# Performance work log

Measured on AMD Instinct MI355X. Metric: run time of the kernel, lower is better.

Reference implementation:

```python
import jax, jax.numpy as jnp
import numpy as np

EPS = 1e-15
BN_EPS = 1e-5
N_NODES = 50000
N_EDGES = 800000
IN_CH = 32
OUT_CH = 32
DIM = 3


def _gmm_params(key, in_ch, out_ch, K):
    k1, k2, k3, k4 = jax.random.split(key, 4)
    g = jax.random.normal(k1, (in_ch, K * out_ch), jnp.float32) * (1.0 / np.sqrt(in_ch))
    mu = jax.random.normal(k2, (K, DIM), jnp.float32)
    sigma = jax.random.uniform(k3, (K, DIM), jnp.float32, 0.5, 1.5)
    root = jax.random.normal(k4, (in_ch, out_ch), jnp.float32) * (1.0 / np.sqrt(in_ch))
    bias = jnp.zeros((out_ch,), jnp.float32)
    return g, mu, sigma, root, bias


def setup_inputs() -> dict:
    key = jax.random.key(0)
    ks = jax.random.split(key, 12)
    x = jax.random.normal(ks[0], (N_NODES, IN_CH), jnp.float32)
    edge_index = jax.random.randint(ks[1], (2, N_EDGES), 0, N_NODES, jnp.int64)
    edge_attr = jax.random.uniform(ks[2], (N_EDGES, DIM), jnp.float32)
    g1, mu1, sig1, root1, b1 = _gmm_params(ks[3], IN_CH, OUT_CH, 5)
    g2, mu2, sig2, root2, b2 = _gmm_params(ks[4], OUT_CH, OUT_CH, 5)
    gs, mus, sigs, roots, bs = _gmm_params(ks[5], IN_CH, OUT_CH, 1)
    ones = jnp.ones((OUT_CH,), jnp.float32)
    zeros = jnp.zeros((OUT_CH,), jnp.float32)
    return dict(x=x, edge_attr=edge_attr,
                g1=g1, mu1=mu1, sig1=sig1, root1=root1, b1=b1, gam1=ones, bet1=zeros,
                g2=g2, mu2=mu2, sig2=sig2, root2=root2, b2=b2, gam2=ones, bet2=zeros,
                gs=gs, mus=mus, sigs=sigs, roots=roots, bs=bs, gams=ones, bets=zeros,
                edge_index=edge_index)


def gmm_conv(x, edge_index, edge_attr, g, mu, sigma, root, bias, num_nodes):
    # PyG GMMConv (separate kernels=False, aggr='mean', root_weight=True)
    src, dst = edge_index[0], edge_index[1]
    K = mu.shape[0]
    out_ch = root.shape[1]
    # Gaussian mixture weights per edge/kernel: [E, K]
    diff = edge_attr[:, None, :] - mu[None, :, :]               # [E, K, D]
    w = jnp.exp(jnp.sum(-0.5 * diff * diff / (EPS + sigma[None] ** 2), axis=-1))
    # Project and gather source features: [E, K, out]
    xj = (x @ g).reshape(-1, K, out_ch)[src] if False else (x[src] @ g).reshape(-1, K, out_ch)
    msg = jnp.einsum('ek,ekc->ec', w, xj)                        # [E, out]
    agg = jax.ops.segment_sum(msg, dst, num_segments=num_nodes)
    cnt = jax.ops.segment_sum(jnp.ones((msg.shape[0],), msg.dtype), dst, num_segments=num_nodes)
    agg = agg / jnp.maximum(cnt, 1.0)[:, None]                   # mean aggregation
    return agg + x @ root + bias


def batch_norm(x, gamma, beta):
    mean = jnp.mean(x, axis=0)
    var = jnp.var(x, axis=0)
    return gamma * (x - mean) * jax.lax.rsqrt(var + BN_EPS) + beta


def reference(x, edge_attr,
              g1, mu1, sig1, root1, b1, gam1, bet1,
              g2, mu2, sig2, root2, b2, gam2, bet2,
              gs, mus, sigs, roots, bs, gams, bets,
              edge_index):
    n = x.shape[0]
    h = jax.nn.elu(batch_norm(gmm_conv(x, edge_index, edge_attr, g1, mu1, sig1, root1, b1, n), gam1, bet1))
    h = batch_norm(gmm_conv(h, edge_index, edge_attr, g2, mu2, sig2, root2, b2, n), gam2, bet2)
    s = batch_norm(gmm_conv(x, edge_index, edge_attr, gs, mus, sigs, roots, bs, n), gams, bets)
    return jax.nn.elu(h + s)
```

## Files before the change

kernel.cpp:

```cpp
#include <hip/hip_runtime.h>
#include <hip/hip_fp16.h>
#include <math.h>

#define NN 50000
#define NE 800000
#define GEPS 1e-15f
#define BN_EPS 1e-5f
#define NB 196
#define LOG2E 1.4426950408889634f
#define NODES_PER_XCD 6250

typedef _Float16 f16x8 __attribute__((ext_vector_type(8)));
typedef float f32x4 __attribute__((ext_vector_type(4)));

__device__ __forceinline__ float2 h2f(unsigned int u) {
    __half2 h = *reinterpret_cast<const __half2*>(&u);
    return __half22float2(h);
}

__global__ void init_kernel(const float* __restrict__ sig1, const float* __restrict__ mu1,
                            const float* __restrict__ sig2, const float* __restrict__ mu2,
                            const float* __restrict__ sigs, const float* __restrict__ mus,
                            float* __restrict__ gc, int* __restrict__ deg,
                            float* __restrict__ stats) {
    int i = blockIdx.x * blockDim.x + threadIdx.x;
    if (i < NN) deg[i] = 0;
    if (blockIdx.x == 0) {
        int t = threadIdx.x;
        stats[t] = 0.f;
        if (t < 11) {
            const float* sg; const float* mu;
            if (t < 5)       { sg = sig1 + t * 3;       mu = mu1 + t * 3; }
            else if (t < 10) { sg = sig2 + (t - 5) * 3; mu = mu2 + (t - 5) * 3; }
            else             { sg = sigs;               mu = mus; }
            float C = 0.f;
            for (int d = 0; d < 3; d++) {
                float sv = sg[d];
                float iv = -0.5f / (GEPS + sv * sv) * LOG2E;
                float m = mu[d];
                gc[t * 8 + d] = iv;
                gc[t * 8 + 3 + d] = -2.f * iv * m;
                C += iv * m * m;
            }
            gc[t * 8 + 6] = C;
            gc[t * 8 + 7] = 0.f;
        }
    }
}

__global__ void rank_kernel(const int* __restrict__ ei, int* __restrict__ deg,
                            int* __restrict__ rankv) {
    int t = blockIdx.x * blockDim.x + threadIdx.x;
    int e0 = t * 4;
    if (e0 >= NE) return;
    int4 dv = *(const int4*)(ei + NE + e0);
    int4 rv;
    rv.x = atomicAdd(&deg[dv.x], 1);
    rv.y = atomicAdd(&deg[dv.y], 1);
    rv.z = atomicAdd(&deg[dv.z], 1);
    rv.w = atomicAdd(&deg[dv.w], 1);
    *(int4*)(rankv + e0) = rv;
}

__global__ void block_reduce_kernel(const int* __restrict__ deg, int* __restrict__ bsum) {
    __shared__ int sh[256];
    int t = threadIdx.x;
    int i = blockIdx.x * 256 + t;
    sh[t] = (i < NN) ? deg[i] : 0;
    __syncthreads();
    for (int off = 128; off > 0; off >>= 1) {
        if (t < off) sh[t] += sh[t + off];
        __syncthreads();
    }
    if (t == 0) bsum[blockIdx.x] = sh[0];
}

__global__ void scan_partials_kernel(int* __restrict__ bsum) {
    __shared__ int sh[256];
    int t = threadIdx.x;
    int v = (t < NB) ? bsum[t] : 0;
    sh[t] = v;
    __syncthreads();
    for (int off = 1; off < 256; off <<= 1) {
        int u = (t >= off) ? sh[t - off] : 0;
        __syncthreads();
        sh[t] += u;
        __syncthreads();
    }
    if (t < NB) bsum[t] = sh[t] - v;
}

__global__ void block_scan_kernel(const int* __restrict__ deg, const int* __restrict__ bsum,
                                  int* __restrict__ rowstart) {
    __shared__ int sh[256];
    int t = threadIdx.x;
    int i = blockIdx.x * 256 + t;
    int v = (i < NN) ? deg[i] : 0;
    sh[t] = v;
    __syncthreads();
    for (int off = 1; off < 256; off <<= 1) {
        int u = (t >= off) ? sh[t - off] : 0;
        __syncthreads();
        sh[t] += u;
        __syncthreads();
    }
    int excl = sh[t] - v + bsum[blockIdx.x];
    if (i < NN) rowstart[i] = excl;
}

__global__ void scatter_xcd(const int* __restrict__ ei, const int* __restrict__ rankv,
                            const int* __restrict__ rowstart, int* __restrict__ perm) {
    const int g = blockIdx.x & 7;
    const int v = blockIdx.x >> 3;
    const int VB = gridDim.x >> 3;
    const int stride = VB * blockDim.x * 4;
    for (int e0 = (v * blockDim.x + threadIdx.x) * 4; e0 < NE; e0 += stride) {
        int4 dv = *(const int4*)(ei + NE + e0);
        int4 rv = *(const int4*)(rankv + e0);
        if (dv.x / NODES_PER_XCD == g) perm[rowstart[dv.x] + rv.x] = e0;
        if (dv.y / NODES_PER_XCD == g) perm[rowstart[dv.y] + rv.y] = e0 + 1;
        if (dv.z / NODES_PER_XCD == g) perm[rowstart[dv.z] + rv.z] = e0 + 2;
        if (dv.w / NODES_PER_XCD == g) perm[rowstart[dv.w] + rv.w] = e0 + 3;
    }
}

__global__ void reorder_build(const int* __restrict__ perm, const int* __restrict__ ei,
                              const float* __restrict__ ea, const float* __restrict__ gc,
                              int4* __restrict__ recA, int4* __restrict__ recB) {
    int t = blockIdx.x * blockDim.x + threadIdx.x;
    int p0 = t * 4;
    if (p0 >= NE) return;
    int4 pv = *(const int4*)(perm + p0);
    int es[4] = {pv.x, pv.y, pv.z, pv.w};

    int   srcs[4];
    float av[4][3];
#pragma unroll
    for (int k = 0; k < 4; k++) {
        int e = es[k];
        srcs[k] = ei[e];
        av[k][0] = ea[e * 3 + 0];
        av[k][1] = ea[e * 3 + 1];
        av[k][2] = ea[e * 3 + 2];
    }

    int4 qa[4], qb[4];
#pragma unroll
    for (int k = 0; k < 4; k++) {
        float a0 = av[k][0], a1 = av[k][1], a2 = av[k][2];
        float s0 = a0 * a0, s1 = a1 * a1, s2 = a2 * a2;
        __half wv[11];
#pragma unroll
        for (int s = 0; s < 11; s++) {
            float ex = gc[s * 8 + 6];
            ex = fmaf(gc[s * 8 + 3], a0, ex);
            ex = fmaf(gc[s * 8 + 4], a1, ex);
            ex = fmaf(gc[s * 8 + 5], a2, ex);
            ex = fmaf(gc[s * 8 + 0], s0, ex);
            ex = fmaf(gc[s * 8 + 1], s1, ex);
            ex = fmaf(gc[s * 8 + 2], s2, ex);
            wv[s] = __float2half(exp2f(ex));
        }
        union UA { struct { int src; __half w[6]; } r; int4 q; } ua;
        ua.r.src = srcs[k];
        ua.r.w[0] = wv[0]; ua.r.w[1] = wv[1]; ua.r.w[2] = wv[2];
        ua.r.w[3] = wv[3]; ua.r.w[4] = wv[4]; ua.r.w[5] = wv[10];
        union UB { struct { int src; __half w[5]; __half pad; } r; int4 q; } ub;
        ub.r.src = srcs[k];
        ub.r.w[0] = wv[5]; ub.r.w[1] = wv[6]; ub.r.w[2] = wv[7];
        ub.r.w[3] = wv[8]; ub.r.w[4] = wv[9]; ub.r.pad = __float2half(0.f);
        qa[k] = ua.q;
        qb[k] = ub.q;
    }
#pragma unroll
    for (int k = 0; k < 4; k++) recA[p0 + k] = qa[k];
#pragma unroll
    for (int k = 0; k < 4; k++) recB[p0 + k] = qb[k];
}

__global__ void projR_kernel(const float* __restrict__ x, const float* __restrict__ root1,
                             const float* __restrict__ b1, const float* __restrict__ roots,
                             const float* __restrict__ bs, __half* __restrict__ xh,
                             float* __restrict__ R1, float* __restrict__ Rs) {
    const int t = threadIdx.x;
    const int col = t & 31;
    const int half_ = (t >> 5) & 1;
    const int rg = t >> 6;
    float w[32];
    const float* rootp = half_ ? roots : root1;
#pragma unroll
    for (int i = 0; i < 32; i++) w[i] = rootp[i * 32 + col];
    float b = half_ ? bs[col] : b1[col];
    float* Rp = half_ ? Rs : R1;
    __shared__ float hs[256];
    for (int n0 = blockIdx.x * 8; n0 < NN; n0 += gridDim.x * 8) {
        float v = x[(size_t)n0 * 32 + t];
        hs[t] = v;
        xh[(size_t)n0 * 32 + t] = __float2half(v);
        __syncthreads();
#pragma unroll
        for (int rr = 0; rr < 2; rr++) {
            int r = rg * 2 + rr;
            float acc = b;
#pragma unroll
            for (int i = 0; i < 32; i++) acc += w[i] * hs[r * 32 + i];
            Rp[(size_t)(n0 + r) * 32 + col] = acc;
        }
        __syncthreads();
    }
}

__global__ void projB2_kernel(const float* __restrict__ c1, const float* __restrict__ stats,
                              const float* __restrict__ gam1, const float* __restrict__ bet1,
                              const float* __restrict__ root2, const float* __restrict__ b2,
                              __half* __restrict__ hh, float* __restrict__ R2) {
    const int t = threadIdx.x;
    const int col = t & 31;
    const int rg = t >> 5;
    __shared__ float sc[32], sf[32];
    if (t < 32) {
        const float invN = 1.0f / (float)NN;
        float m = stats[t] * invN;
        float v = stats[32 + t] * invN - m * m;
        float s = gam1[t] * rsqrtf(v + BN_EPS);
        sc[t] = s;
        sf[t] = bet1[t] - m * s;
    }
    float w[32];
#pragma unroll
    for (int i = 0; i < 32; i++) w[i] = root2[i * 32 + col];
    float b = b2[col];
    __shared__ float hs[256];
    __syncthreads();
    for (int n0 = blockIdx.x * 8; n0 < NN; n0 += gridDim.x * 8) {
        float v = c1[(size_t)n0 * 32 + t];
        float hv = sc[t & 31] * v + sf[t & 31];
        hv = hv > 0.f ? hv : (__expf(hv) - 1.f);
        hs[t] = hv;
        hh[(size_t)n0 * 32 + t] = __float2half(hv);
        __syncthreads();
        float acc = b;
#pragma unroll
        for (int i = 0; i < 32; i++) acc += w[i] * hs[rg * 32 + i];
        R2[(size_t)(n0 + rg) * 32 + col] = acc;
        __syncthreads();
    }
}

template <bool SKIP>
__global__ void agg_kernel(const int4* __restrict__ rec, const int* __restrict__ rowstart,
                           const int* __restrict__ deg, const __half* __restrict__ X,
                           __half* __restrict__ Aout) {
    constexpr int NS = SKIP ? 6 : 5;
    constexpr int SA = SKIP ? 192 : 160;
    const int tid = blockIdx.x * blockDim.x + threadIdx.x;
    const int lane = threadIdx.x & 63;
    const int grp = lane >> 4;
    const int ch2 = lane & 15;
    const int wavesTotal = (gridDim.x * blockDim.x) >> 6;
    const int wid = tid >> 6;

    for (int n = wid; n < NN; n += wavesTotal) {
        const int start = rowstart[n];
        const int d = deg[n];
        float2 acc[NS];
#pragma unroll
        for (int s = 0; s < NS; s++) acc[s] = make_float2(0.f, 0.f);
        int i = grp;
        for (; i + 4 < d; i += 8) {
            int4 r0 = rec[(size_t)(start + i)];
            int4 r1 = rec[(size_t)(start + i + 4)];
            const __half2 xv0 = *(const __half2*)(X + (((size_t)r0.x) << 5) + 2 * ch2);
            const __half2 xv1 = *(const __half2*)(X + (((size_t)r1.x) << 5) + 2 * ch2);
            float2 xf0 = __half22float2(xv0);
            float2 xf1 = __half22float2(xv1);
            {
                float2 w01 = h2f((unsigned)r0.y);
                float2 w23 = h2f((unsigned)r0.z);
                float2 w45 = h2f((unsigned)r0.w);
                float wv[6] = {w01.x, w01.y, w23.x, w23.y, w45.x, w45.y};
#pragma unroll
                for (int s = 0; s < NS; s++) {
                    acc[s].x = fmaf(wv[s], xf0.x, acc[s].x);
                    acc[s].y = fmaf(wv[s], xf0.y, acc[s].y);
                }
            }
            {
                float2 w01 = h2f((unsigned)r1.y);
                float2 w23 = h2f((unsigned)r1.z);
                float2 w45 = h2f((unsigned)r1.w);
                float wv[6] = {w01.x, w01.y, w23.x, w23.y, w45.x, w45.y};
#pragma unroll
                for (int s = 0; s < NS; s++) {
                    acc[s].x = fmaf(wv[s], xf1.x, acc[s].x);
                    acc[s].y = fmaf(wv[s], xf1.y, acc[s].y);
                }
            }
        }
        if (i < d) {
            int4 r = rec[(size_t)(start + i)];
            const __half2 xv = *(const __half2*)(X + (((size_t)r.x) << 5) + 2 * ch2);
            float2 xf = __half22float2(xv);
            float2 w01 = h2f((unsigned)r.y);
            float2 w23 = h2f((unsigned)r.z);
            float2 w45 = h2f((unsigned)r.w);
            float wv[6] = {w01.x, w01.y, w23.x, w23.y, w45.x, w45.y};
#pragma unroll
            for (int s = 0; s < NS; s++) {
                acc[s].x = fmaf(wv[s], xf.x, acc[s].x);
                acc[s].y = fmaf(wv[s], xf.y, acc[s].y);
            }
        }
#pragma unroll
        for (int s = 0; s < NS; s++) {
            acc[s].x += __shfl_xor(acc[s].x, 16, 64);
            acc[s].x += __shfl_xor(acc[s].x, 32, 64);
            acc[s].y += __shfl_xor(acc[s].y, 16, 64);
            acc[s].y += __shfl_xor(acc[s].y, 32, 64);
        }
        if (grp == 0) {
            const float invd = 1.0f / fmaxf((float)d, 1.0f);
            __half* base = Aout + (size_t)n * SA + 2 * ch2;
#pragma unroll
            for (int s = 0; s < 5; s++) {
                __half2 hv = __floats2half2_rn(acc[s].x * invd, acc[s].y * invd);
                *(__half2*)(base + s * 32) = hv;
            }
            if (SKIP) {
                __half2 hv = __floats2half2_rn(acc[5].x * invd, acc[5].y * invd);
                *(__half2*)(base + 160) = hv;
            }
        }
    }
}

template <bool SKIP>
__global__ __launch_bounds__(256, 4) void gemm_kernel(
        const __half* __restrict__ Ah, const float* __restrict__ G,
        const float* __restrict__ Gs, const float* __restrict__ R,
        const float* __restrict__ Rs, float* __restrict__ C,
        float* __restrict__ Cs, float* __restrict__ stats) {
    constexpr int SA = SKIP ? 192 : 160;
    const int tid = blockIdx.x * blockDim.x + threadIdx.x;
    const int l = threadIdx.x & 63;
    const int r16 = l & 15;
    const int quad = l >> 4;
    const int wid = tid >> 6;
    const int nw = (gridDim.x * blockDim.x) >> 6;

    f16x8 bf[5][2];
#pragma unroll
    for (int kt = 0; kt < 5; kt++)
#pragma unroll
        for (int ct = 0; ct < 2; ct++)
#pragma unroll
            for (int e = 0; e < 8; e++) {
                int jj = quad * 8 + e;
                bf[kt][ct][e] = (_Float16)G[jj * 160 + kt * 32 + ct * 16 + r16];
            }
    f16x8 bs[2];
    if (SKIP) {
#pragma unroll
        for (int ct = 0; ct < 2; ct++)
#pragma unroll
            for (int e = 0; e < 8; e++) {
                int jj = quad * 8 + e;
                bs[ct][e] = (_Float16)Gs[jj * 32 + ct * 16 + r16];
            }
    }

    float s0 = 0.f, s1 = 0.f, q0 = 0.f, q1 = 0.f;
    float t0 = 0.f, t1 = 0.f, u0 = 0.f, u1 = 0.f;

    for (int tile = wid; tile < NN / 16; tile += nw) {
        const int n0 = tile * 16;
        const __half* arow = Ah + (size_t)(n0 + r16) * SA + quad * 8;
        f32x4 acc0 = {0.f, 0.f, 0.f, 0.f};
        f32x4 acc1 = {0.f, 0.f, 0.f, 0.f};
        f32x4 sa0 = {0.f, 0.f, 0.f, 0.f};
        f32x4 sa1 = {0.f, 0.f, 0.f, 0.f};
#pragma unroll
        for (int kt = 0; kt < 5; kt++) {
            f16x8 a = *(const f16x8*)(arow + kt * 32);
            acc0 = __builtin_amdgcn_mfma_f32_16x16x32_f16(a, bf[kt][0], acc0, 0, 0, 0);
            acc1 = __builtin_amdgcn_mfma_f32_16x16x32_f16(a, bf[kt][1], acc1, 0, 0, 0);
        }
        if (SKIP) {
            f16x8 a = *(const f16x8*)(arow + 160);
            sa0 = __builtin_amdgcn_mfma_f32_16x16x32_f16(a, bs[0], sa0, 0, 0, 0);
            sa1 = __builtin_amdgcn_mfma_f32_16x16x32_f16(a, bs[1], sa1, 0, 0, 0);
        }
#pragma unroll
        for (int r = 0; r < 4; r++) {
            const int nr = n0 + quad * 4 + r;
            const int b = nr * 32;
            {
                float v = acc0[r] + R[b + r16];
                C[b + r16] = v; s0 += v; q0 += v * v;
            }
            {
                float v = acc1[r] + R[b + 16 + r16];
                C[b + 16 + r16] = v; s1 += v; q1 += v * v;
            }
            if (SKIP) {
                float v = sa0[r] + Rs[b + r16];
                Cs[b + r16] = v; t0 += v; u0 += v * v;
                float w2 = sa1[r] + Rs[b + 16 + r16];
                Cs[b + 16 + r16] = w2; t1 += w2; u1 += w2 * w2;
            }
        }
    }
    s0 += __shfl_xor(s0, 16, 64); s0 += __shfl_xor(s0, 32, 64);
    s1 += __shfl_xor(s1, 16, 64); s1 += __shfl_xor(s1, 32, 64);
    q0 += __shfl_xor(q0, 16, 64); q0 += __shfl_xor(q0, 32, 64);
    q1 += __shfl_xor(q1, 16, 64); q1 += __shfl_xor(q1, 32, 64);
    if (SKIP) {
        t0 += __shfl_xor(t0, 16, 64); t0 += __shfl_xor(t0, 32, 64);
        t1 += __shfl_xor(t1, 16, 64); t1 += __shfl_xor(t1, 32, 64);
        u0 += __shfl_xor(u0, 16, 64); u0 += __shfl_xor(u0, 32, 64);
        u1 += __shfl_xor(u1, 16, 64); u1 += __shfl_xor(u1, 32, 64);
    }
    __shared__ float sred[128];
    const int t = threadIdx.x;
    if (t < 128) sred[t] = 0.f;
    __syncthreads();
    if (l < 16) {
        atomicAdd(&sred[l], s0);       atomicAdd(&sred[16 + l], s1);
        atomicAdd(&sred[32 + l], q0);  atomicAdd(&sred[48 + l], q1);
        if (SKIP) {
            atomicAdd(&sred[64 + l], t0);  atomicAdd(&sred[80 + l], t1);
            atomicAdd(&sred[96 + l], u0);  atomicAdd(&sred[112 + l], u1);
        }
    }
    __syncthreads();
    if (SKIP) { if (t < 128) atomicAdd(&stats[t], sred[t]); }
    else      { if (t < 64)  atomicAdd(&stats[t], sred[t]); }
}

__global__ void apply2_kernel(const float* __restrict__ c2, const float* __restrict__ cs,
                              const float* __restrict__ stats, const float* __restrict__ gam2,
                              const float* __restrict__ bet2, const float* __restrict__ gams,
                              const float* __restrict__ bets, float* __restrict__ out) {
    int idx = blockIdx.x * blockDim.x + threadIdx.x;
    if (idx >= NN * 32) return;
    int ch = idx & 31;
    const float invN = 1.0f / (float)NN;
    float m2 = stats[128 + ch] * invN;
    float v2 = stats[160 + ch] * invN - m2 * m2;
    float ms = stats[64 + ch] * invN;
    float vs = stats[96 + ch] * invN - ms * ms;
    float bn2 = gam2[ch] * (c2[idx] - m2) * rsqrtf(v2 + BN_EPS) + bet2[ch];
    float bns = gams[ch] * (cs[idx] - ms) * rsqrtf(vs + BN_EPS) + bets[ch];
    float o = bn2 + bns;
    out[idx] = o > 0.f ? o : (__expf(o) - 1.f);
}

extern "C" void kernel_launch(void* const* d_in, const int* in_sizes, int n_in,
                              void* d_out, int out_size, void* d_ws, size_t ws_size,
                              hipStream_t stream) {
    const float* x     = (const float*)d_in[0];
    const float* ea    = (const float*)d_in[1];
    const float* g1    = (const float*)d_in[2];
    const float* mu1   = (const float*)d_in[3];
    const float* sig1  = (const float*)d_in[4];
    const float* root1 = (const float*)d_in[5];
    const float* b1    = (const float*)d_in[6];
    const float* gam1  = (const float*)d_in[7];
    const float* bet1  = (const float*)d_in[8];
    const float* g2    = (const float*)d_in[9];
    const float* mu2   = (const float*)d_in[10];
    const float* sig2  = (const float*)d_in[11];
    const float* root2 = (const float*)d_in[12];
    const float* b2    = (const float*)d_in[13];
    const float* gam2  = (const float*)d_in[14];
    const float* bet2  = (const float*)d_in[15];
    const float* gs    = (const float*)d_in[16];
    const float* mus   = (const float*)d_in[17];
    const float* sigs  = (const float*)d_in[18];
    const float* roots = (const float*)d_in[19];
    const float* bs    = (const float*)d_in[20];
    const float* gams  = (const float*)d_in[21];
    const float* bets  = (const float*)d_in[22];
    const int*   ei    = (const int*)d_in[23];
    float* out = (float*)d_out;

    char* w = (char*)d_ws;
    __half* xh  = (__half*)w;   w += (size_t)NN * 32 * 2;
    __half* hh  = (__half*)w;   w += (size_t)NN * 32 * 2;
    __half* Ah  = (__half*)w;   w += (size_t)NN * 192 * 2;
    float*  R1  = (float*)w;    w += (size_t)NN * 32 * 4;
    float*  Rs  = (float*)w;    w += (size_t)NN * 32 * 4;
    float*  R2  = (float*)w;    w += (size_t)NN * 32 * 4;
    float*  c1  = (float*)w;    w += (size_t)NN * 32 * 4;
    float*  cs  = (float*)w;    w += (size_t)NN * 32 * 4;
    int4*   recA = (int4*)w;    w += (size_t)NE * 16;
    int4*   recB = (int4*)w;    w += (size_t)NE * 16;
    int*    perm = (int*)w;     w += (size_t)NE * 4;
    int*    rankv = (int*)w;    w += (size_t)NE * 4;
    int*    deg = (int*)w;      w += (size_t)NN * 4;
    int*    rowstart = (int*)w; w += (size_t)NN * 4;
    int*    bsum = (int*)w;     w += 256 * 4;
    float*  stats = (float*)w;  w += 256 * 4;
    float*  gc    = (float*)w;  w += 11 * 8 * 4;

    const int ilpBlocks   = (NE / 4 + 255) / 256;
    const int applyBlocks = (NN * 32 + 255) / 256;

    init_kernel<<<NB, 256, 0, stream>>>(sig1, mu1, sig2, mu2, sigs, mus, gc, deg, stats);

    rank_kernel<<<ilpBlocks, 256, 0, stream>>>(ei, deg, rankv);
    block_reduce_kernel<<<NB, 256, 0, stream>>>(deg, bsum);
    scan_partials_kernel<<<1, 256, 0, stream>>>(bsum);
    block_scan_kernel<<<NB, 256, 0, stream>>>(deg, bsum, rowstart);
    scatter_xcd<<<1024, 256, 0, stream>>>(ei, rankv, rowstart, perm);
    reorder_build<<<ilpBlocks, 256, 0, stream>>>(perm, ei, ea, gc, recA, recB);

    projR_kernel<<<1024, 256, 0, stream>>>(x, root1, b1, roots, bs, xh, R1, Rs);
    agg_kernel<true><<<2048, 256, 0, stream>>>(recA, rowstart, deg, xh, Ah);
    gemm_kernel<true><<<512, 256, 0, stream>>>(Ah, g1, gs, R1, Rs, c1, cs, stats);

    projB2_kernel<<<1024, 256, 0, stream>>>(c1, stats, gam1, bet1, root2, b2, hh, R2);
    agg_kernel<false><<<2048, 256, 0, stream>>>(recB, rowstart, deg, hh, Ah);
    gemm_kernel<false><<<512, 256, 0, stream>>>(Ah, g2, nullptr, R2, nullptr, c1, nullptr,
                                                stats + 128);
    apply2_kernel<<<applyBlocks, 256, 0, stream>>>(c1, cs, stats, gam2, bet2, gams, bets, out);
}
```

Baseline: 298.4 us.

## Merge degree scan into one kernel and fuse root projection with edge scatter

The three-kernel block reduce/scan/scan sequence that builds rowstart is replaced by a single 1024-thread block: each thread serially sums a chunk of about 49 degrees, the block scans those sums in shared memory, then each thread writes its chunk's exclusive offsets. The root projection kernel is folded into the edge scatter kernel as 512 extra blocks, so the compute-light projection can overlap the atomic-free scatter writes. Together this removes three kernel launches and their serialization gaps. The risk is that the single-block scan is serial and reads deg with strided per-thread chunks, and the 512 projection blocks now cover the nodes with a fixed stride instead of 1024 blocks.

Result: slower. 376.7 us (+26.3%).

```diff
diff --git a/kernel.cpp b/kernel.cpp
--- a/kernel.cpp
+++ b/kernel.cpp
@@ -6,7 +6,6 @@
 #define NE 800000
 #define GEPS 1e-15f
 #define BN_EPS 1e-5f
-#define NB 196
 #define LOG2E 1.4426950408889634f
 #define NODES_PER_XCD 6250
 
@@ -62,65 +61,81 @@
     *(int4*)(rankv + e0) = rv;
 }
 
-__global__ void block_reduce_kernel(const int* __restrict__ deg, int* __restrict__ bsum) {
-    __shared__ int sh[256];
-    int t = threadIdx.x;
-    int i = blockIdx.x * 256 + t;
-    sh[t] = (i < NN) ? deg[i] : 0;
+__global__ void scan_kernel(const int* __restrict__ deg, int* __restrict__ rowstart) {
+    __shared__ int sh[1024];
+    const int t = threadIdx.x;
+    const int per = (NN + 1023) / 1024;
+    const int base = t * per;
+    int sum = 0;
+    for (int k = 0; k < per; k++) {
+        int idx = base + k;
+        if (idx < NN) sum += deg[idx];
+    }
+    sh[t] = sum;
     __syncthreads();
-    for (int off = 128; off > 0; off >>= 1) {
-        if (t < off) sh[t] += sh[t + off];
-        __syncthreads();
-    }
-    if (t == 0) bsum[blockIdx.x] = sh[0];
-}
-
-__global__ void scan_partials_kernel(int* __restrict__ bsum) {
-    __shared__ int sh[256];
-    int t = threadIdx.x;
-    int v = (t < NB) ? bsum[t] : 0;
-    sh[t] = v;
-    __syncthreads();
-    for (int off = 1; off < 256; off <<= 1) {
+    for (int off = 1; off < 1024; off <<= 1) {
         int u = (t >= off) ? sh[t - off] : 0;
         __syncthreads();
         sh[t] += u;
         __syncthreads();
     }
-    if (t < NB) bsum[t] = sh[t] - v;
-}
-
-__global__ void block_scan_kernel(const int* __restrict__ deg, const int* __restrict__ bsum,
-                                  int* __restrict__ rowstart) {
-    __shared__ int sh[256];
-    int t = threadIdx.x;
-    int i = blockIdx.x * 256 + t;
-    int v = (i < NN) ? deg[i] : 0;
-    sh[t] = v;
-    __syncthreads();
-    for (int off = 1; off < 256; off <<= 1) {
-        int u = (t >= off) ? sh[t - off] : 0;
-        __syncthreads();
-        sh[t] += u;
-        __syncthreads();
-    }
-    int excl = sh[t] - v + bsum[blockIdx.x];
-    if (i < NN) rowstart[i] = excl;
-}
-
-__global__ void scatter_xcd(const int* __restrict__ ei, const int* __restrict__ rankv,
-                            const int* __restrict__ rowstart, int* __restrict__ perm) {
-    const int g = blockIdx.x & 7;
-    const int v = blockIdx.x >> 3;
-    const int VB = gridDim.x >> 3;
-    const int stride = VB * blockDim.x * 4;
-    for (int e0 = (v * blockDim.x + threadIdx.x) * 4; e0 < NE; e0 += stride) {
-        int4 dv = *(const int4*)(ei + NE + e0);
-        int4 rv = *(const int4*)(rankv + e0);
-        if (dv.x / NODES_PER_XCD == g) perm[rowstart[dv.x] + rv.x] = e0;
-        if (dv.y / NODES_PER_XCD == g) perm[rowstart[dv.y] + rv.y] = e0 + 1;
-        if (dv.z / NODES_PER_XCD == g) perm[rowstart[dv.z] + rv.z] = e0 + 2;
-        if (dv.w / NODES_PER_XCD == g) perm[rowstart[dv.w] + rv.w] = e0 + 3;
+    int run = sh[t] - sum;
+    for (int k = 0; k < per; k++) {
+        int idx = base + k;
+        if (idx < NN) {
+            rowstart[idx] = run;
+            run += deg[idx];
+        }
+    }
+}
+
+__global__ void scatter_proj_kernel(const int* __restrict__ ei, const int* __restrict__ rankv,
+                                    const int* __restrict__ rowstart, int* __restrict__ perm,
+                                    const float* __restrict__ x, const float* __restrict__ root1,
+                                    const float* __restrict__ b1, const float* __restrict__ roots,
+                                    const float* __restrict__ bs, __half* __restrict__ xh,
+                                    float* __restrict__ R1, float* __restrict__ Rs) {
+    if (blockIdx.x < 1024) {
+        const int g = blockIdx.x & 7;
+        const int v = blockIdx.x >> 3;
+        const int VB = 1024 >> 3;
+        const int stride = VB * blockDim.x * 4;
+        for (int e0 = (v * blockDim.x + threadIdx.x) * 4; e0 < NE; e0 += stride) {
+            int4 dv = *(const int4*)(ei + NE + e0);
+            int4 rv = *(const int4*)(rankv + e0);
+            if (dv.x / NODES_PER_XCD == g) perm[rowstart[dv.x] + rv.x] = e0;
+            if (dv.y / NODES_PER_XCD == g) perm[rowstart[dv.y] + rv.y] = e0 + 1;
+            if (dv.z / NODES_PER_XCD == g) perm[rowstart[dv.z] + rv.z] = e0 + 2;
+            if (dv.w / NODES_PER_XCD == g) perm[rowstart[dv.w] + rv.w] = e0 + 3;
+        }
+    } else {
+        const int pb = blockIdx.x - 1024;
+        const int t = threadIdx.x;
+        const int col = t & 31;
+        const int half_ = (t >> 5) & 1;
+        const int rg = t >> 6;
+        float w[32];
+        const float* rootp = half_ ? roots : root1;
+#pragma unroll
+        for (int i = 0; i < 32; i++) w[i] = rootp[i * 32 + col];
+        float b = half_ ? bs[col] : b1[col];
+        float* Rp = half_ ? Rs : R1;
+        __shared__ float hs[256];
+        for (int n0 = pb * 8; n0 < NN; n0 += 512 * 8) {
+            float v = x[(size_t)n0 * 32 + t];
+            hs[t] = v;
+            xh[(size_t)n0 * 32 + t] = __float2half(v);
+            __syncthreads();
+#pragma unroll
+            for (int rr = 0; rr < 2; rr++) {
+                int r = rg * 2 + rr;
+                float acc = b;
+#pragma unroll
+                for (int i = 0; i < 32; i++) acc += w[i] * hs[r * 32 + i];
+                Rp[(size_t)(n0 + r) * 32 + col] = acc;
+            }
+            __syncthreads();
+        }
     }
 }
 
@@ -176,38 +191,6 @@
     for (int k = 0; k < 4; k++) recA[p0 + k] = qa[k];
 #pragma unroll
     for (int k = 0; k < 4; k++) recB[p0 + k] = qb[k];
-}
-
-__global__ void projR_kernel(const float* __restrict__ x, const float* __restrict__ root1,
-                             const float* __restrict__ b1, const float* __restrict__ roots,
-                             const float* __restrict__ bs, __half* __restrict__ xh,
-                             float* __restrict__ R1, float* __restrict__ Rs) {
-    const int t = threadIdx.x;
-    const int col = t & 31;
-    const int half_ = (t >> 5) & 1;
-    const int rg = t >> 6;
-    float w[32];
-    const float* rootp = half_ ? roots : root1;
-#pragma unroll
-    for (int i = 0; i < 32; i++) w[i] = rootp[i * 32 + col];
-    float b = half_ ? bs[col] : b1[col];
-    float* Rp = half_ ? Rs : R1;
-    __shared__ float hs[256];
-    for (int n0 = blockIdx.x * 8; n0 < NN; n0 += gridDim.x * 8) {
-        float v = x[(size_t)n0 * 32 + t];
-        hs[t] = v;
-        xh[(size_t)n0 * 32 + t] = __float2half(v);
-        __syncthreads();
-#pragma unroll
-        for (int rr = 0; rr < 2; rr++) {
-            int r = rg * 2 + rr;
-            float acc = b;
-#pragma unroll
-            for (int i = 0; i < 32; i++) acc += w[i] * hs[r * 32 + i];
-            Rp[(size_t)(n0 + r) * 32 + col] = acc;
-        }
-        __syncthreads();
-    }
 }
 
 __global__ void projB2_kernel(const float* __restrict__ c1, const float* __restrict__ stats,
@@ -499,23 +482,21 @@
     int*    rankv = (int*)w;    w += (size_t)NE * 4;
     int*    deg = (int*)w;      w += (size_t)NN * 4;
     int*    rowstart = (int*)w; w += (size_t)NN * 4;
-    int*    bsum = (int*)w;     w += 256 * 4;
     float*  stats = (float*)w;  w += 256 * 4;
     float*  gc    = (float*)w;  w += 11 * 8 * 4;
 
     const int ilpBlocks   = (NE / 4 + 255) / 256;
     const int applyBlocks = (NN * 32 + 255) / 256;
-
-    init_kernel<<<NB, 256, 0, stream>>>(sig1, mu1, sig2, mu2, sigs, mus, gc, deg, stats);
+    const int NBinit      = (NN + 255) / 256;
+
+    init_kernel<<<NBinit, 256, 0, stream>>>(sig1, mu1, sig2, mu2, sigs, mus, gc, deg, stats);
 
     rank_kernel<<<ilpBlocks, 256, 0, stream>>>(ei, deg, rankv);
-    block_reduce_kernel<<<NB, 256, 0, stream>>>(deg, bsum);
-    scan_partials_kernel<<<1, 256, 0, stream>>>(bsum);
-    block_scan_kernel<<<NB, 256, 0, stream>>>(deg, bsum, rowstart);
-    scatter_xcd<<<1024, 256, 0, stream>>>(ei, rankv, rowstart, perm);
+    scan_kernel<<<1, 1024, 0, stream>>>(deg, rowstart);
+    scatter_proj_kernel<<<1536, 256, 0, stream>>>(ei, rankv, rowstart, perm,
+                                                  x, root1, b1, roots, bs, xh, R1, Rs);
     reorder_build<<<ilpBlocks, 256, 0, stream>>>(perm, ei, ea, gc, recA, recB);
 
-    projR_kernel<<<1024, 256, 0, stream>>>(x, root1, b1, roots, bs, xh, R1, Rs);
     agg_kernel<true><<<2048, 256, 0, stream>>>(recA, rowstart, deg, xh, Ah);
     gemm_kernel<true><<<512, 256, 0, stream>>>(Ah, g1, gs, R1, Rs, c1, cs, stats);
 
```
